# Performance work log

Hardware: AMD Instinct MI355X
Metric: run time of the kernel (lower is better)

## Reference

```python
import jax, jax.numpy as jnp
import numpy as np

N = 100000        # unique nodes in batch (node_num)
IN_DIM = 256
OUT_DIM = 128
E_RAND = 1_600_000  # random graph edges (avg degree 16)
B = N             # batch nodes (all nodes, each gets a self-loop edge)
SLOPE = 0.1       # leaky_relu slope_ratio


def setup_inputs() -> dict:
    key = jax.random.key(0)
    k1, k2, k3, k4, k5, k6 = jax.random.split(key, 6)
    x = jax.random.normal(k1, (N, IN_DIM), dtype=jnp.float32)
    # small weight scale keeps exp(leaky_relu(.)) in a sane range, like kaiming on unit-ish inputs
    W = jax.random.normal(k2, (OUT_DIM, IN_DIM), dtype=jnp.float32) * 0.05
    b = jax.random.normal(k3, (OUT_DIM,), dtype=jnp.float32) * 0.05
    a = jax.random.normal(k4, (2 * OUT_DIM, 1), dtype=jnp.float32) * 0.05
    src = jax.random.randint(k5, (E_RAND,), 0, N, dtype=jnp.int32)
    dst = jax.random.randint(k6, (E_RAND,), 0, N, dtype=jnp.int32)
    batch_idx = jnp.arange(B, dtype=jnp.int32)
    # append self-loop edges for every batch node (original vstacks original_node_edge)
    edges = jnp.stack([jnp.concatenate([src, batch_idx]),
                       jnp.concatenate([dst, batch_idx])], axis=1)  # [E_TOT, 2]
    return {"x": x, "W": W, "b": b, "a": a, "edges": edges, "batch_idx": batch_idx}


def reference(x, W, b, a, edges, batch_idx):
    # new_embeddings = Linear(in_dim -> out_dim)
    emb = x @ W.T + b  # [N, out_dim]
    # concat(h_src, h_dst) @ a  ==  h_src @ a[:d] + h_dst @ a[d:]
    a1 = a[:OUT_DIM, 0]
    a2 = a[OUT_DIM:, 0]
    s_src = emb @ a1  # [N]
    s_dst = emb @ a2  # [N]
    src, dst = edges[:, 0], edges[:, 1]
    logits = s_src[src] + s_dst[dst]                                 # [E]
    score = jnp.exp(jax.nn.leaky_relu(logits, negative_slope=SLOPE))  # [E]
    # sparse row-sum and aggregation fused as segment reductions over src
    row_sum = jax.ops.segment_sum(score, src, num_segments=N)        # [N]
    msgs = score[:, None] * emb[dst]                                 # [E, out_dim]
    results = jax.ops.segment_sum(msgs, src, num_segments=N)         # [N, out_dim]
    # nodes with no outgoing edges have row_sum==0; they are never gathered below
    safe_rs = jnp.where(row_sum > 0, row_sum, 1.0)
    out = results / safe_rs[:, None]
    return out[batch_idx]
```

## Files before the change

### kernel.cpp

```cpp
#include <hip/hip_runtime.h>
#include <hip/hip_fp16.h>

#define IN_DIM 256
#define OUT_DIM 128
#define SLOPE 0.1f

typedef __attribute__((ext_vector_type(8))) short short8;
typedef __attribute__((ext_vector_type(4))) float f32x4;

__device__ __forceinline__ unsigned bf16_rne(float f) {
    unsigned u = __float_as_uint(f);
    return (u + 0x7FFFu + ((u >> 16) & 1u)) >> 16;
}

__global__ __launch_bounds__(256) void wsplit_kernel(
    const float* __restrict__ W, short* __restrict__ Whi, short* __restrict__ Wlo)
{
    const int i = blockIdx.x * 256 + threadIdx.x;
    const float v = W[i];
    const unsigned hb = bf16_rne(v);
    const float hf = __uint_as_float(hb << 16);
    Whi[i] = (short)hb;
    Wlo[i] = (short)bf16_rne(v - hf);
}

__global__ __launch_bounds__(256) void gemm_emb_kernel(
    const float* __restrict__ x, const short* __restrict__ Whi_g,
    const short* __restrict__ Wlo_g, const float* __restrict__ bias,
    const float* __restrict__ a, __half* __restrict__ emb_h,
    float* __restrict__ s1, float* __restrict__ s2, int N)
{
    __shared__ short lds[12288];
    short* Ahi = lds;
    short* Alo = lds + 2048;
    short* Bhi = lds + 4096;
    short* Blo = lds + 8192;

    const int tid = threadIdx.x;
    const int l   = tid & 63;
    const int w   = tid >> 6;
    const int gm0 = blockIdx.x * 64;

    const int arow = tid >> 2;
    const int akc  = tid & 3;
    const int gmA  = gm0 + arow;
    const bool av_ok = (gmA < N);
    const int brow = tid >> 1;
    const int bkc0 = (tid & 1) * 2;

    f32x4 acc[8];
    #pragma unroll
    for (int j = 0; j < 8; ++j) acc[j] = (f32x4)0.f;

    float bias_v[8], av1[8], av2[8];
    #pragma unroll
    for (int nf = 0; nf < 8; ++nf) {
        const int col = nf * 16 + (l & 15);
        bias_v[nf] = bias[col];
        av1[nf]    = a[col];
        av2[nf]    = a[OUT_DIM + col];
    }

    for (int ks = 0; ks < 8; ++ks) {
        const int k0 = ks * 32;
        {
            float v[8];
            if (av_ok) {
                const float4 p0 = *(const float4*)&x[(size_t)gmA * IN_DIM + k0 + akc * 8];
                const float4 p1 = *(const float4*)&x[(size_t)gmA * IN_DIM + k0 + akc * 8 + 4];
                v[0]=p0.x; v[1]=p0.y; v[2]=p0.z; v[3]=p0.w;
                v[4]=p1.x; v[5]=p1.y; v[6]=p1.z; v[7]=p1.w;
            } else {
                #pragma unroll
                for (int j = 0; j < 8; ++j) v[j] = 0.f;
            }
            short8 h8, l8;
            #pragma unroll
            for (int j = 0; j < 8; ++j) {
                unsigned hb = bf16_rne(v[j]);
                float hf = __uint_as_float(hb << 16);
                h8[j] = (short)hb;
                l8[j] = (short)bf16_rne(v[j] - hf);
            }
            *(short8*)&Ahi[akc * 512 + arow * 8] = h8;
            *(short8*)&Alo[akc * 512 + arow * 8] = l8;
        }
        #pragma unroll
        for (int q = 0; q < 2; ++q) {
            const int kc = bkc0 + q;
            const short8 h8 = *(const short8*)&Whi_g[brow * IN_DIM + k0 + kc * 8];
            const short8 l8 = *(const short8*)&Wlo_g[brow * IN_DIM + k0 + kc * 8];
            *(short8*)&Bhi[kc * 1024 + brow * 8] = h8;
            *(short8*)&Blo[kc * 1024 + brow * 8] = l8;
        }
        __syncthreads();

        const int arow_f = w * 16 + (l & 15);
        const int aoff   = (l >> 4) * 512 + arow_f * 8;
        const short8 ah = *(const short8*)&Ahi[aoff];
        const short8 al = *(const short8*)&Alo[aoff];
        #pragma unroll
        for (int nf = 0; nf < 8; ++nf) {
            const int col = nf * 16 + (l & 15);
            const int boff = (l >> 4) * 1024 + col * 8;
            const short8 bh = *(const short8*)&Bhi[boff];
            const short8 bl = *(const short8*)&Blo[boff];
            acc[nf] = __builtin_amdgcn_mfma_f32_16x16x32_bf16(ah, bh, acc[nf], 0, 0, 0);
            acc[nf] = __builtin_amdgcn_mfma_f32_16x16x32_bf16(al, bh, acc[nf], 0, 0, 0);
            acc[nf] = __builtin_amdgcn_mfma_f32_16x16x32_bf16(ah, bl, acc[nf], 0, 0, 0);
        }
        __syncthreads();
    }

    __half* hl = (__half*)lds;
    #pragma unroll
    for (int r = 0; r < 4; ++r) {
        const int lrow = w * 16 + (l >> 4) * 4 + r;
        float p1 = 0.f, p2 = 0.f;
        #pragma unroll
        for (int nf = 0; nf < 8; ++nf) {
            const float e = acc[nf][r] + bias_v[nf];
            p1 += e * av1[nf];
            p2 += e * av2[nf];
            hl[lrow * 144 + nf * 16 + (l & 15)] = __float2half(e);
        }
        p1 += __shfl_xor(p1, 1); p1 += __shfl_xor(p1, 2);
        p1 += __shfl_xor(p1, 4); p1 += __shfl_xor(p1, 8);
        p2 += __shfl_xor(p2, 1); p2 += __shfl_xor(p2, 2);
        p2 += __shfl_xor(p2, 4); p2 += __shfl_xor(p2, 8);
        const int gm = gm0 + lrow;
        if ((l & 15) == 0 && gm < N) { s1[gm] = p1; s2[gm] = p2; }
    }
    __syncthreads();
    #pragma unroll
    for (int i = 0; i < 4; ++i) {
        const int idx = i * 256 + tid;
        const int row = idx >> 4, seg = idx & 15;
        if (gm0 + row < N) {
            const uint4 u = *(const uint4*)&hl[row * 144 + seg * 8];
            ((uint4*)emb_h)[(size_t)(gm0 + row) * 16 + seg] = u;
        }
    }
}

__global__ __launch_bounds__(256) void rank_kernel(
    const int* __restrict__ edges, int* __restrict__ deg,
    int* __restrict__ rank, int E)
{
    const int e0 = (blockIdx.x * 256 + threadIdx.x) * 4;
    if (e0 + 3 < E) {
        const int4 ea = ((const int4*)edges)[(e0 >> 1) + 0];
        const int4 eb = ((const int4*)edges)[(e0 >> 1) + 1];
        const int r0 = atomicAdd(&deg[ea.x], 1);
        const int r1 = atomicAdd(&deg[ea.z], 1);
        const int r2 = atomicAdd(&deg[eb.x], 1);
        const int r3 = atomicAdd(&deg[eb.z], 1);
        ((int4*)rank)[e0 >> 2] = make_int4(r0, r1, r2, r3);
    } else if (e0 < E) {
        for (int e = e0; e < E; ++e) {
            const int2 ed = ((const int2*)edges)[e];
            rank[e] = atomicAdd(&deg[ed.x], 1);
        }
    }
}

__global__ __launch_bounds__(256) void scan1_kernel(
    const int* __restrict__ deg, int* __restrict__ off,
    int* __restrict__ bsum, int N)
{
    __shared__ int lds[256];
    const int t = threadIdx.x;
    const int base = blockIdx.x * 1024 + t * 4;
    int v[4];
    int ts = 0;
    #pragma unroll
    for (int j = 0; j < 4; ++j) {
        v[j] = (base + j < N) ? deg[base + j] : 0;
        ts += v[j];
    }
    lds[t] = ts;
    __syncthreads();
    for (int d = 1; d < 256; d <<= 1) {
        int xv = (t >= d) ? lds[t - d] : 0;
        __syncthreads();
        lds[t] += xv;
        __syncthreads();
    }
    int run = lds[t] - ts;
    #pragma unroll
    for (int j = 0; j < 4; ++j) {
        if (base + j < N) off[base + j] = run;
        run += v[j];
    }
    if (t == 255) bsum[blockIdx.x] = lds[255];
}

__global__ __launch_bounds__(256) void scan3_kernel(
    int* __restrict__ off, const int* __restrict__ bsum,
    const int* __restrict__ bidx, int* __restrict__ flag, int N, int E)
{
    __shared__ int red[256];
    const int t = threadIdx.x;
    const int chunk = (int)(blockIdx.x >> 2);
    int s = 0;
    for (int j = t; j < chunk; j += 256) s += bsum[j];
    red[t] = s;
    __syncthreads();
    #pragma unroll
    for (int d = 128; d > 0; d >>= 1) {
        if (t < d) red[t] += red[t + d];
        __syncthreads();
    }
    const int pref = red[0];
    const int i = blockIdx.x * 256 + t;
    if (i < N) {
        off[i] += pref;
        if (bidx[i] != i) atomicOr(flag, 1);
    }
    if (i == 0) off[N] = E;
}

__global__ __launch_bounds__(256) void fill_kernel(
    const int* __restrict__ edges, const int* __restrict__ off,
    const int* __restrict__ rank, int* __restrict__ csr, int E)
{
    const int e0 = (blockIdx.x * 256 + threadIdx.x) * 4;
    if (e0 + 3 < E) {
        const int4 ea = ((const int4*)edges)[(e0 >> 1) + 0];
        const int4 eb = ((const int4*)edges)[(e0 >> 1) + 1];
        const int4 rk = ((const int4*)rank)[e0 >> 2];
        csr[off[ea.x] + rk.x] = ea.y;
        csr[off[ea.z] + rk.y] = ea.w;
        csr[off[eb.x] + rk.z] = eb.y;
        csr[off[eb.z] + rk.w] = eb.w;
    } else if (e0 < E) {
        for (int e = e0; e < E; ++e) {
            const int2 ed = ((const int2*)edges)[e];
            csr[off[ed.x] + rank[e]] = ed.y;
        }
    }
}

__global__ __launch_bounds__(256) void agg_kernel(
    const int* __restrict__ off, const int* __restrict__ csr,
    const float* __restrict__ s1, const float* __restrict__ s2,
    const __half* __restrict__ emb_h, const int* __restrict__ flag,
    float* __restrict__ results, float* __restrict__ out, int N)
{
    __shared__ int2 sl[4][64];

    const int wid  = (int)((blockIdx.x * 256u + threadIdx.x) >> 6);
    const int lane = threadIdx.x & 63;
    const int wv   = threadIdx.x >> 6;
    if (wid >= N) return;
    const int eg = lane >> 4;
    const int cl = lane & 15;
    const int beg = off[wid];
    const int end = off[wid + 1];
    const float s1n = s1[wid];

    const float4* __restrict__ embrow = (const float4*)emb_h;
    int2* slot = &sl[wv][0];

    float av[8];
    #pragma unroll
    for (int k = 0; k < 8; ++k) av[k] = 0.f;
    float rsl = 0.f;

    for (int tile = beg; tile < end; tile += 64) {
        const int cnt = min(64, end - tile);
        int d = 0; float sc = 0.f;
        if (lane < cnt) {
            d = csr[tile + lane];
            const float ll = s1n + s2[d];
            sc = __expf(ll > 0.f ? ll : SLOPE * ll);
        }
        rsl += sc;
        slot[lane] = make_int2(d, __float_as_int(sc));
        __builtin_amdgcn_wave_barrier();
        for (int j0 = 0; j0 < cnt; j0 += 32) {
            const int nq = ((cnt - j0) + 3) >> 2;
            int dq[8]; float scq[8];
            #pragma unroll
            for (int q = 0; q < 8; ++q) {
                dq[q] = 0; scq[q] = 0.f;
                if (q < nq) {
                    const int2 p = slot[j0 + q * 4 + eg];
                    dq[q] = p.x; scq[q] = __int_as_float(p.y);
                }
            }
            float4 vq[8];
            #pragma unroll
            for (int q = 0; q < 8; ++q)
                if (q < nq) vq[q] = embrow[(size_t)dq[q] * 16 + cl];
            #pragma unroll
            for (int q = 0; q < 8; ++q) {
                if (q < nq) {
                    const __half* hp = reinterpret_cast<const __half*>(&vq[q]);
                    #pragma unroll
                    for (int k = 0; k < 8; ++k)
                        av[k] += scq[q] * __half2float(hp[k]);
                }
            }
        }
        __builtin_amdgcn_wave_barrier();
    }

    float rs = rsl;
    rs += __shfl_xor(rs, 1);  rs += __shfl_xor(rs, 2);
    rs += __shfl_xor(rs, 4);  rs += __shfl_xor(rs, 8);
    rs += __shfl_xor(rs, 16); rs += __shfl_xor(rs, 32);
    #pragma unroll
    for (int k = 0; k < 8; ++k) {
        av[k] += __shfl_xor(av[k], 16);
        av[k] += __shfl_xor(av[k], 32);
    }

    const float inv = 1.f / (rs > 0.f ? rs : 1.f);
    if (eg == 0) {
        float* dbuf = (*flag == 0) ? out : results;
        float4* rp = (float4*)&dbuf[(size_t)wid * 128 + cl * 8];
        rp[0] = make_float4(av[0] * inv, av[1] * inv, av[2] * inv, av[3] * inv);
        rp[1] = make_float4(av[4] * inv, av[5] * inv, av[6] * inv, av[7] * inv);
    }
}

__global__ __launch_bounds__(256) void gather_kernel(
    const float* __restrict__ results, const int* __restrict__ bidx,
    const int* __restrict__ flag, float* __restrict__ out, int N)
{
    if (*flag == 0) return;
    const unsigned i = blockIdx.x * 256u + threadIdx.x;
    if (i >= (unsigned)N * 32u) return;
    const unsigned n = i >> 5, c = i & 31;
    ((float4*)out)[i] = ((const float4*)results)[(size_t)bidx[n] * 32 + c];
}

extern "C" void kernel_launch(void* const* d_in, const int* in_sizes, int n_in,
                              void* d_out, int out_size, void* d_ws, size_t ws_size,
                              hipStream_t stream) {
    const float* x     = (const float*)d_in[0];
    const float* W     = (const float*)d_in[1];
    const float* b     = (const float*)d_in[2];
    const float* a     = (const float*)d_in[3];
    const int*   edges = (const int*)d_in[4];
    const int*   bidx  = (const int*)d_in[5];

    const int N = in_sizes[5];
    const int E = in_sizes[4] / 2;

    float*  results = (float*)d_ws;
    __half* emb_h   = (__half*)(results + (size_t)N * OUT_DIM);
    int*    rank    = (int*)(emb_h + (size_t)N * OUT_DIM);
    int*    csr     = rank + E;
    float*  s1      = (float*)(csr + E);
    float*  s2      = s1 + N;
    int*    deg     = (int*)(s2 + N);
    int*    flag    = deg + N;
    int*    off     = flag + 1;
    int*    bsum    = off + N + 1;
    short*  Whi     = (short*)(bsum + 256);
    short*  Wlo     = Whi + OUT_DIM * IN_DIM;

    hipMemsetAsync(deg, 0, (size_t)(N + 1) * sizeof(int), stream);

    wsplit_kernel<<<(OUT_DIM * IN_DIM) / 256, 256, 0, stream>>>(W, Whi, Wlo);

    dim3 gGemm((N + 63) / 64);
    gemm_emb_kernel<<<gGemm, 256, 0, stream>>>(x, Whi, Wlo, b, a, emb_h, s1, s2, N);

    const int gE4 = (E / 4 + 255) / 256 + 1;
    rank_kernel<<<gE4, 256, 0, stream>>>(edges, deg, rank, E);

    const int nb = (N + 1023) / 1024;
    scan1_kernel<<<nb, 256, 0, stream>>>(deg, off, bsum, N);
    scan3_kernel<<<(N + 255) / 256, 256, 0, stream>>>(off, bsum, bidx, flag, N, E);

    fill_kernel<<<gE4, 256, 0, stream>>>(edges, off, rank, csr, E);

    const unsigned aggThreads = (unsigned)N * 64u;
    agg_kernel<<<(aggThreads + 255u) / 256u, 256, 0, stream>>>(
        off, csr, s1, s2, emb_h, flag, results, (float*)d_out, N);

    const unsigned gatherThreads = (unsigned)N * 32u;
    gather_kernel<<<(gatherThreads + 255u) / 256u, 256, 0, stream>>>(
        results, bidx, flag, (float*)d_out, N);
}
```

Measured before the change: 225.1 us.

## Fuse edge rank atomic counting into the embedding GEMM kernel

Moves the per-edge degree-counting atomics (rank computation) into the GEMM kernel, interleaving one edge per thread per K-step with the MFMA work, with a tail kernel for edges beyond the fused capacity. The aim is to overlap the latency-bound atomic traffic with compute-bound GEMM and remove a separate kernel launch. In exchange it adds register pressure, extra global loads and atomics inside the GEMM loop, and a fully unrolled K loop.

```diff
diff --git a/kernel.cpp b/kernel.cpp
--- a/kernel.cpp
+++ b/kernel.cpp
@@ -28,7 +28,9 @@
     const float* __restrict__ x, const short* __restrict__ Whi_g,
     const short* __restrict__ Wlo_g, const float* __restrict__ bias,
     const float* __restrict__ a, __half* __restrict__ emb_h,
-    float* __restrict__ s1, float* __restrict__ s2, int N)
+    float* __restrict__ s1, float* __restrict__ s2,
+    const int* __restrict__ edges, int* __restrict__ deg,
+    int* __restrict__ rank, int N, int E, int ept)
 {
     __shared__ short lds[12288];
     short* Ahi = lds;
@@ -40,6 +42,12 @@
     const int l   = tid & 63;
     const int w   = tid >> 6;
     const int gm0 = blockIdx.x * 64;
+
+    const int gtid = blockIdx.x * 256 + tid;
+    const int T    = (int)gridDim.x * 256;
+    int rnk[8];
+    #pragma unroll
+    for (int i = 0; i < 8; ++i) rnk[i] = 0;
 
     const int arow = tid >> 2;
     const int akc  = tid & 3;
@@ -61,6 +69,10 @@
         av2[nf]    = a[OUT_DIM + col];
     }
 
+    int src_cur = 0;
+    if (0 < ept && gtid < E) src_cur = edges[2 * (size_t)gtid];
+
+    #pragma unroll
     for (int ks = 0; ks < 8; ++ks) {
         const int k0 = ks * 32;
         {
@@ -95,6 +107,17 @@
         }
         __syncthreads();
 
+        int src_nxt = 0;
+        if (ks + 1 < ept) {
+            const int en = gtid + (ks + 1) * T;
+            if (en < E) src_nxt = edges[2 * (size_t)en];
+        }
+        if (ks < ept) {
+            const int e = gtid + ks * T;
+            if (e < E) rnk[ks] = atomicAdd(&deg[src_cur], 1);
+        }
+        src_cur = src_nxt;
+
         const int arow_f = w * 16 + (l & 15);
         const int aoff   = (l >> 4) * 512 + arow_f * 8;
         const short8 ah = *(const short8*)&Ahi[aoff];
@@ -141,27 +164,24 @@
             ((uint4*)emb_h)[(size_t)(gm0 + row) * 16 + seg] = u;
         }
     }
-}
-
-__global__ __launch_bounds__(256) void rank_kernel(
+
+    #pragma unroll
+    for (int i = 0; i < 8; ++i) {
+        if (i < ept) {
+            const int e = gtid + i * T;
+            if (e < E) rank[e] = rnk[i];
+        }
+    }
+}
+
+__global__ __launch_bounds__(256) void rank_tail_kernel(
     const int* __restrict__ edges, int* __restrict__ deg,
-    int* __restrict__ rank, int E)
-{
-    const int e0 = (blockIdx.x * 256 + threadIdx.x) * 4;
-    if (e0 + 3 < E) {
-        const int4 ea = ((const int4*)edges)[(e0 >> 1) + 0];
-        const int4 eb = ((const int4*)edges)[(e0 >> 1) + 1];
-        const int r0 = atomicAdd(&deg[ea.x], 1);
-        const int r1 = atomicAdd(&deg[ea.z], 1);
-        const int r2 = atomicAdd(&deg[eb.x], 1);
-        const int r3 = atomicAdd(&deg[eb.z], 1);
-        ((int4*)rank)[e0 >> 2] = make_int4(r0, r1, r2, r3);
-    } else if (e0 < E) {
-        for (int e = e0; e < E; ++e) {
-            const int2 ed = ((const int2*)edges)[e];
-            rank[e] = atomicAdd(&deg[ed.x], 1);
-        }
-    }
+    int* __restrict__ rank, int e0base, int E)
+{
+    const int e = e0base + blockIdx.x * 256 + threadIdx.x;
+    if (e >= E) return;
+    const int2 ed = ((const int2*)edges)[e];
+    rank[e] = atomicAdd(&deg[ed.x], 1);
 }
 
 __global__ __launch_bounds__(256) void scan1_kernel(
@@ -366,16 +386,25 @@
 
     wsplit_kernel<<<(OUT_DIM * IN_DIM) / 256, 256, 0, stream>>>(W, Whi, Wlo);
 
-    dim3 gGemm((N + 63) / 64);
-    gemm_emb_kernel<<<gGemm, 256, 0, stream>>>(x, Whi, Wlo, b, a, emb_h, s1, s2, N);
-
-    const int gE4 = (E / 4 + 255) / 256 + 1;
-    rank_kernel<<<gE4, 256, 0, stream>>>(edges, deg, rank, E);
+    const int nGemm   = (N + 63) / 64;
+    const int threads = nGemm * 256;
+    int ept = (E + threads - 1) / threads;
+    if (ept > 8) ept = 8;
+    gemm_emb_kernel<<<nGemm, 256, 0, stream>>>(
+        x, Whi, Wlo, b, a, emb_h, s1, s2, edges, deg, rank, N, E, ept);
+
+    const long long cap = (long long)threads * 8;
+    if ((long long)E > cap) {
+        const int tailE = E - (int)cap;
+        rank_tail_kernel<<<(tailE + 255) / 256, 256, 0, stream>>>(
+            edges, deg, rank, (int)cap, E);
+    }
 
     const int nb = (N + 1023) / 1024;
     scan1_kernel<<<nb, 256, 0, stream>>>(deg, off, bsum, N);
     scan3_kernel<<<(N + 255) / 256, 256, 0, stream>>>(off, bsum, bidx, flag, N, E);
 
+    const int gE4 = (E / 4 + 255) / 256 + 1;
     fill_kernel<<<gE4, 256, 0, stream>>>(edges, off, rank, csr, E);
 
     const unsigned aggThreads = (unsigned)N * 64u;
```

New measurement: 213.4 us. -5.2%, faster.

## Fuse edge rank counting into GEMM launch as dedicated leading blocks

Applied to the files above, without the earlier changes.

The separate rank kernel is merged into the GEMM kernel. The first 64 blocks each process a contiguous span of edges with atomic degree counting, and the remaining blocks do the embedding GEMM. This lets the latency-bound atomic pass overlap with the compute-bound GEMM and removes one launch. The tradeoff is that only 64 blocks do the atomic work serially over large spans, so it could become a tail that outlasts the GEMM blocks.

```diff
diff --git a/kernel.cpp b/kernel.cpp
--- a/kernel.cpp
+++ b/kernel.cpp
@@ -24,13 +24,39 @@
     Wlo[i] = (short)bf16_rne(v - hf);
 }
 
-__global__ __launch_bounds__(256) void gemm_emb_kernel(
+__global__ __launch_bounds__(256) void gemm_rank_kernel(
     const float* __restrict__ x, const short* __restrict__ Whi_g,
     const short* __restrict__ Wlo_g, const float* __restrict__ bias,
     const float* __restrict__ a, __half* __restrict__ emb_h,
-    float* __restrict__ s1, float* __restrict__ s2, int N)
+    float* __restrict__ s1, float* __restrict__ s2,
+    const int* __restrict__ edges, int* __restrict__ deg,
+    int* __restrict__ rank, int N, int E, int nRank, int span)
 {
     __shared__ short lds[12288];
+
+    if ((int)blockIdx.x < nRank) {
+        const int rb   = (int)blockIdx.x;
+        const int base = rb * span;
+        const int endb = min(base + span, E);
+        for (int e0 = base + (int)threadIdx.x * 4; e0 < endb; e0 += 1024) {
+            if (e0 + 3 < endb) {
+                const int4 ea = ((const int4*)edges)[(e0 >> 1) + 0];
+                const int4 eb = ((const int4*)edges)[(e0 >> 1) + 1];
+                const int r0 = atomicAdd(&deg[ea.x], 1);
+                const int r1 = atomicAdd(&deg[ea.z], 1);
+                const int r2 = atomicAdd(&deg[eb.x], 1);
+                const int r3 = atomicAdd(&deg[eb.z], 1);
+                ((int4*)rank)[e0 >> 2] = make_int4(r0, r1, r2, r3);
+            } else {
+                for (int e = e0; e < endb; ++e) {
+                    const int2 ed = ((const int2*)edges)[e];
+                    rank[e] = atomicAdd(&deg[ed.x], 1);
+                }
+            }
+        }
+        return;
+    }
+
     short* Ahi = lds;
     short* Alo = lds + 2048;
     short* Bhi = lds + 4096;
@@ -39,7 +65,7 @@
     const int tid = threadIdx.x;
     const int l   = tid & 63;
     const int w   = tid >> 6;
-    const int gm0 = blockIdx.x * 64;
+    const int gm0 = ((int)blockIdx.x - nRank) * 64;
 
     const int arow = tid >> 2;
     const int akc  = tid & 3;
@@ -143,27 +169,6 @@
     }
 }
 
-__global__ __launch_bounds__(256) void rank_kernel(
-    const int* __restrict__ edges, int* __restrict__ deg,
-    int* __restrict__ rank, int E)
-{
-    const int e0 = (blockIdx.x * 256 + threadIdx.x) * 4;
-    if (e0 + 3 < E) {
-        const int4 ea = ((const int4*)edges)[(e0 >> 1) + 0];
-        const int4 eb = ((const int4*)edges)[(e0 >> 1) + 1];
-        const int r0 = atomicAdd(&deg[ea.x], 1);
-        const int r1 = atomicAdd(&deg[ea.z], 1);
-        const int r2 = atomicAdd(&deg[eb.x], 1);
-        const int r3 = atomicAdd(&deg[eb.z], 1);
-        ((int4*)rank)[e0 >> 2] = make_int4(r0, r1, r2, r3);
-    } else if (e0 < E) {
-        for (int e = e0; e < E; ++e) {
-            const int2 ed = ((const int2*)edges)[e];
-            rank[e] = atomicAdd(&deg[ed.x], 1);
-        }
-    }
-}
-
 __global__ __launch_bounds__(256) void scan1_kernel(
     const int* __restrict__ deg, int* __restrict__ off,
     int* __restrict__ bsum, int N)
@@ -366,16 +371,17 @@
 
     wsplit_kernel<<<(OUT_DIM * IN_DIM) / 256, 256, 0, stream>>>(W, Whi, Wlo);
 
-    dim3 gGemm((N + 63) / 64);
-    gemm_emb_kernel<<<gGemm, 256, 0, stream>>>(x, Whi, Wlo, b, a, emb_h, s1, s2, N);
-
-    const int gE4 = (E / 4 + 255) / 256 + 1;
-    rank_kernel<<<gE4, 256, 0, stream>>>(edges, deg, rank, E);
+    const int nRank = 64;
+    const int span  = (((E + nRank - 1) / nRank) + 3) & ~3;
+    const int nGemm = (N + 63) / 64;
+    gemm_rank_kernel<<<nRank + nGemm, 256, 0, stream>>>(
+        x, Whi, Wlo, b, a, emb_h, s1, s2, edges, deg, rank, N, E, nRank, span);
 
     const int nb = (N + 1023) / 1024;
     scan1_kernel<<<nb, 256, 0, stream>>>(deg, off, bsum, N);
     scan3_kernel<<<(N + 255) / 256, 256, 0, stream>>>(off, bsum, bidx, flag, N, E);
 
+    const int gE4 = (E / 4 + 255) / 256 + 1;
     fill_kernel<<<gE4, 256, 0, stream>>>(edges, off, rank, csr, E);
 
     const unsigned aggThreads = (unsigned)N * 64u;
```

Result: faster. 203.3 us (-9.7%).
